# Kernel tuning notes

Measured on AMD Instinct MI355X. Metric: run time of the kernel, lower is better.

Reference implementation:

```python
import jax, jax.numpy as jnp
import numpy as np

# ---- structural constants (mirror e3nn SO3.tensor_productRs bookkeeping) ----
MUL = 2                      # multiplicity of every irrep in Rs_in / Rs_out
LS = [0, 1, 2]               # irrep orders present in Rs_in and Rs_out
L_MAX = 2                    # spherical-harmonics cutoff -> Y_dim = 9
N_BASIS, HIDDEN = 64, 64     # radial model sizes
R_MAX, GAMMA = 3.5, 4.0      # gaussian radial basis params


def _filter_paths():
    """One entry (l_filter) per (mul_out, mul_in, l_in, l_out, l_f) path."""
    paths = []
    for l_in in LS:
        for l_out in LS:
            for lf in range(abs(l_in - l_out), min(l_in + l_out, L_MAX) + 1):
                paths.extend([lf] * (MUL * MUL))  # mul_in * mul_out copies
    return paths  # len == n_path == 60


def _build_mix_matrices():
    """rf_mix[K, n_path]: broadcast each radial path weight over its 2l+1 components.
    ylm_mix[K, 9]: select Y_{l,m} for each filter component. Both 0/1, block sparse."""
    paths = _filter_paths()
    n_path = len(paths)
    K = sum(2 * l + 1 for l in paths)          # 204
    y_off = {0: 0, 1: 1, 2: 4}                 # offset of l-block inside Y (dim 9)
    rf = np.zeros((K, n_path), dtype=np.float32)
    ylm = np.zeros((K, 9), dtype=np.float32)
    k = 0
    for p, l in enumerate(paths):
        for m in range(2 * l + 1):
            rf[k, p] = 1.0
            ylm[k, y_off[l] + m] = 1.0
            k += 1
    return rf, ylm, n_path, K


def _sh_l012(n):
    """Real spherical harmonics l=0..2 on unit vectors n[Z,3] -> Y[9, Z]."""
    x, y, z = n[:, 0], n[:, 1], n[:, 2]
    c0 = 0.28209479177387814   # 1/(2 sqrt(pi))
    c1 = 0.4886025119029199    # sqrt(3/(4 pi))
    c2a = 1.0925484305920792   # sqrt(15/(4 pi))
    c2b = 0.31539156525252005  # sqrt(5/(16 pi))
    c2c = 0.5462742152960396   # sqrt(15/(16 pi))
    one = jnp.ones_like(x)
    return jnp.stack([
        c0 * one,
        c1 * y, c1 * z, c1 * x,
        c2a * x * y, c2a * y * z, c2b * (3.0 * z * z - 1.0), c2a * x * z,
        c2c * (x * x - y * y),
    ], axis=0)


def setup_inputs() -> dict:
    key = jax.random.key(0)
    k_r, k_cg, k_w1, k_w2 = jax.random.split(key, 4)
    Z = 65536
    D = MUL * sum(2 * l + 1 for l in LS)       # 18 (dim_in == dim_out)
    rf_np, ylm_np, n_path, K = _build_mix_matrices()
    r = 2.0 * jax.random.normal(k_r, (Z, 3), dtype=jnp.float32)
    cg = jax.random.normal(k_cg, (K, D, D), dtype=jnp.float32) / np.sqrt(K)
    W1 = jax.random.normal(k_w1, (N_BASIS, HIDDEN), dtype=jnp.float32) / np.sqrt(N_BASIS)
    b1 = jnp.zeros((HIDDEN,), dtype=jnp.float32)
    W2 = jax.random.normal(k_w2, (HIDDEN, n_path), dtype=jnp.float32) / np.sqrt(HIDDEN)
    b2 = jnp.zeros((n_path,), dtype=jnp.float32)
    return {"r": r, "W1": W1, "b1": b1, "W2": W2, "b2": b2,
            "cg": cg, "rf_mix": jnp.asarray(rf_np), "ylm_mix": jnp.asarray(ylm_np)}


def reference(r, W1, b1, W2, b2, cg, rf_mix, ylm_mix):
    radii = jnp.linalg.norm(r, axis=1)                    # [Z]
    n = r / (radii[:, None] + 1e-12)                      # unit directions
    Y = _sh_l012(n)                                       # [9, Z]  (sh returns [m, ...])
    centers = jnp.linspace(0.0, R_MAX, N_BASIS, dtype=jnp.float32)
    B = jnp.exp(-GAMMA * (radii[:, None] - centers) ** 2) # gaussian radial basis [Z, 64]
    R = jax.nn.relu(B @ W1 + b1) @ W2 + b2                # RadialModel -> [Z, n_path]
    Rm = jnp.einsum('kp,zp->zk', rf_mix, R)               # 'ij,zj->zi'
    Ym = jnp.einsum('ky,yz->zk', ylm_mix, Y)              # 'ij,jz->zi'
    # 'kij,zk,zk->zij' : fuse the two per-point vectors, then one GEMM over k
    kernel = jnp.einsum('kij,zk->zij', cg, Rm * Ym)       # [Z, 18, 18]
    return kernel
```

## Files before the change

kernel.cpp:

```cpp
#include <hip/hip_runtime.h>

#define NPATH 60
#define KDIM  204
#define KPAD  224
#define NIJ   324
#define NTIL  21
#define HID   64

typedef short bf16x8 __attribute__((ext_vector_type(8)));
typedef float f32x4  __attribute__((ext_vector_type(4)));

__device__ __align__(16) unsigned short g_w1s[4096];
__device__ __align__(16) unsigned short g_w2s[4096];
__device__ __align__(16) unsigned short g_cgs[75264];
__device__ unsigned char g_ptab[KDIM];
__device__ unsigned char g_ytab[KDIM];

__device__ inline unsigned short f2bf(float f) {
    unsigned int u = __builtin_bit_cast(unsigned int, f);
    u += 0x7fffu + ((u >> 16) & 1u);
    return (unsigned short)(u >> 16);
}
__device__ inline float bf2f(unsigned short h) {
    unsigned int u = ((unsigned int)h) << 16;
    return __builtin_bit_cast(float, u);
}

__global__ void prep_kernel(const float* __restrict__ W1, const float* __restrict__ W2,
                            const float* __restrict__ cg, const float* __restrict__ rf,
                            const float* __restrict__ ylm)
{
    int idx = blockIdx.x * 256 + threadIdx.x;
    if (idx < 4096) {
        int e = idx & 7, ln = (idx >> 3) & 63, nt = (idx >> 9) & 3, kc = idx >> 11;
        int k = kc * 32 + (ln >> 4) * 8 + e;
        int n = nt * 16 + (ln & 15);
        g_w1s[idx] = f2bf(W1[k * HID + n]);
    } else if (idx < 8192) {
        int j = idx - 4096;
        int e = j & 7, ln = (j >> 3) & 63, nt = (j >> 9) & 3, kc = j >> 11;
        int k = kc * 32 + (ln >> 4) * 8 + e;
        int n = nt * 16 + (ln & 15);
        g_w2s[j] = f2bf(n < NPATH ? W2[k * NPATH + n] : 0.0f);
    } else if (idx < 8192 + 75264) {
        int j = idx - 8192;
        int e = j & 7, ln = (j >> 3) & 63;
        int nt = (j >> 9) % NTIL;
        int kc = j / (512 * NTIL);
        int k = kc * 32 + (ln >> 4) * 8 + e;
        int n = nt * 16 + (ln & 15);
        g_cgs[j] = f2bf((k < KDIM && n < NIJ) ? cg[k * NIJ + n] : 0.0f);
    } else if (idx < 8192 + 75264 + KDIM) {
        int k = idx - (8192 + 75264);
        int p = 0, yy = 0;
        for (int q = 0; q < NPATH; q++) if (rf[k * NPATH + q] != 0.0f) p = q;
        for (int q = 0; q < 9; q++)     if (ylm[k * 9 + q]   != 0.0f) yy = q;
        g_ptab[k] = (unsigned char)p;
        g_ytab[k] = (unsigned char)yy;
    }
}

union SmemU {
    struct {
        unsigned short Blds[64][72];
        unsigned short Hlds[64][72];
    } p1;
    unsigned short Clds[64][228];
    float stage[16][340];
};

__global__ __launch_bounds__(256) void fused_kernel(
    const float* __restrict__ r, const float* __restrict__ b1,
    const float* __restrict__ b2, float* __restrict__ out)
{
    __shared__ SmemU sm;
    __shared__ unsigned short Rl[64][61];
    __shared__ float Yl[64][9];
    __shared__ float radl[64];
    __shared__ unsigned char ptabL[KDIM];
    __shared__ unsigned char ytabL[KDIM];

    const int tid  = threadIdx.x;
    const int wv   = tid >> 6;
    const int lane = tid & 63;
    const int quad = lane >> 4;
    const int l16  = lane & 15;
    const int z0   = blockIdx.x * 64;

    if (tid < 64) {
        int z = z0 + tid;
        float x = r[z * 3 + 0], y = r[z * 3 + 1], zc = r[z * 3 + 2];
        float rad = sqrtf(x * x + y * y + zc * zc);
        float inv = 1.0f / (rad + 1e-12f);
        float nx = x * inv, ny = y * inv, nz = zc * inv;
        radl[tid] = rad;
        const float c0 = 0.28209479177387814f, c1 = 0.4886025119029199f;
        const float c2a = 1.0925484305920792f, c2b = 0.31539156525252005f, c2c = 0.5462742152960396f;
        Yl[tid][0] = c0;
        Yl[tid][1] = c1 * ny;
        Yl[tid][2] = c1 * nz;
        Yl[tid][3] = c1 * nx;
        Yl[tid][4] = c2a * nx * ny;
        Yl[tid][5] = c2a * ny * nz;
        Yl[tid][6] = c2b * (3.0f * nz * nz - 1.0f);
        Yl[tid][7] = c2a * nx * nz;
        Yl[tid][8] = c2c * (nx * nx - ny * ny);
    }
    for (int k = tid; k < KDIM; k += 256) {
        ptabL[k] = g_ptab[k];
        ytabL[k] = g_ytab[k];
    }
    __syncthreads();

    {
        int zz = tid >> 2, grp = tid & 3;
        float rad = radl[zz];
        unsigned int* dst = (unsigned int*)&sm.p1.Blds[zz][grp * 16];
        const float step = 3.5f / 63.0f;
        #pragma unroll
        for (int ii = 0; ii < 8; ii++) {
            int i0 = grp * 16 + ii * 2;
            float d0 = rad - (float)i0 * step;
            float d1 = rad - (float)(i0 + 1) * step;
            unsigned int u0 = f2bf(expf(-4.0f * d0 * d0));
            unsigned int u1 = f2bf(expf(-4.0f * d1 * d1));
            dst[ii] = u0 | (u1 << 16);
        }
    }
    __syncthreads();

    {
        bf16x8 a0 = *(const bf16x8*)&sm.p1.Blds[wv * 16 + l16][0 + quad * 8];
        bf16x8 a1 = *(const bf16x8*)&sm.p1.Blds[wv * 16 + l16][32 + quad * 8];
        #pragma unroll
        for (int nt = 0; nt < 4; nt++) {
            bf16x8 bb0 = *(const bf16x8*)&g_w1s[((0 * 4 + nt) * 64 + lane) * 8];
            bf16x8 bb1 = *(const bf16x8*)&g_w1s[((1 * 4 + nt) * 64 + lane) * 8];
            f32x4 acc = {0.f, 0.f, 0.f, 0.f};
            acc = __builtin_amdgcn_mfma_f32_16x16x32_bf16(a0, bb0, acc, 0, 0, 0);
            acc = __builtin_amdgcn_mfma_f32_16x16x32_bf16(a1, bb1, acc, 0, 0, 0);
            int h = nt * 16 + l16;
            float bias = b1[h];
            #pragma unroll
            for (int rr = 0; rr < 4; rr++) {
                float v = acc[rr] + bias;
                v = v > 0.0f ? v : 0.0f;
                sm.p1.Hlds[wv * 16 + quad * 4 + rr][h] = f2bf(v);
            }
        }
    }
    __syncthreads();

    {
        bf16x8 a0 = *(const bf16x8*)&sm.p1.Hlds[wv * 16 + l16][0 + quad * 8];
        bf16x8 a1 = *(const bf16x8*)&sm.p1.Hlds[wv * 16 + l16][32 + quad * 8];
        #pragma unroll
        for (int nt = 0; nt < 4; nt++) {
            bf16x8 bb0 = *(const bf16x8*)&g_w2s[((0 * 4 + nt) * 64 + lane) * 8];
            bf16x8 bb1 = *(const bf16x8*)&g_w2s[((1 * 4 + nt) * 64 + lane) * 8];
            f32x4 acc = {0.f, 0.f, 0.f, 0.f};
            acc = __builtin_amdgcn_mfma_f32_16x16x32_bf16(a0, bb0, acc, 0, 0, 0);
            acc = __builtin_amdgcn_mfma_f32_16x16x32_bf16(a1, bb1, acc, 0, 0, 0);
            int p = nt * 16 + l16;
            if (p < NPATH) {
                float bias = b2[p];
                #pragma unroll
                for (int rr = 0; rr < 4; rr++)
                    Rl[wv * 16 + quad * 4 + rr][p] = f2bf(acc[rr] + bias);
            }
        }
    }
    __syncthreads();

    for (int idx = tid; idx < 64 * (KPAD / 2); idx += 256) {
        int z = idx / (KPAD / 2);
        int k = (idx % (KPAD / 2)) * 2;
        unsigned int u = 0;
        if (k < KDIM) {
            float cA = bf2f(Rl[z][ptabL[k]])     * Yl[z][ytabL[k]];
            float cB = bf2f(Rl[z][ptabL[k + 1]]) * Yl[z][ytabL[k + 1]];
            u = (unsigned int)f2bf(cA) | ((unsigned int)f2bf(cB) << 16);
        }
        *(unsigned int*)&sm.Clds[z][k] = u;
    }
    __syncthreads();

    const int ntb = wv * 5 + (wv > 0 ? 1 : 0);
    const int cnt = (wv == 0) ? 6 : 5;

    f32x4 acc[6][4];
    #pragma unroll
    for (int i = 0; i < 6; i++)
        #pragma unroll
        for (int zt = 0; zt < 4; zt++)
            acc[i][zt] = (f32x4){0.f, 0.f, 0.f, 0.f};

    #pragma unroll
    for (int kc = 0; kc < 7; kc++) {
        bf16x8 az[4];
        #pragma unroll
        for (int zt = 0; zt < 4; zt++)
            az[zt] = *(const bf16x8*)&sm.Clds[zt * 16 + l16][kc * 32 + quad * 8];

        bf16x8 bg[6];
        #pragma unroll
        for (int i = 0; i < 6; i++) {
            int nt = ntb + i; if (nt > NTIL - 1) nt = NTIL - 1;
            bg[i] = *(const bf16x8*)&g_cgs[((kc * NTIL + nt) * 64 + lane) * 8];
        }
        #pragma unroll
        for (int i = 0; i < 6; i++) {
            if (i < cnt) {
                #pragma unroll
                for (int zt = 0; zt < 4; zt++)
                    acc[i][zt] = __builtin_amdgcn_mfma_f32_16x16x32_bf16(az[zt], bg[i], acc[i][zt], 0, 0, 0);
            }
        }
    }

    for (int zt = 0; zt < 4; zt++) {
        __syncthreads();
        #pragma unroll
        for (int i = 0; i < 6; i++) {
            if (i < cnt) {
                int col = (ntb + i) * 16 + l16;
                #pragma unroll
                for (int rr = 0; rr < 4; rr++)
                    sm.stage[quad * 4 + rr][col] = acc[i][zt][rr];
            }
        }
        __syncthreads();
        for (int j = tid; j < 16 * (NIJ / 4); j += 256) {
            int row = j / (NIJ / 4);
            int c4  = j % (NIJ / 4);
            f32x4 v = *(const f32x4*)&sm.stage[row][c4 * 4];
            *(f32x4*)&out[(z0 + zt * 16 + row) * NIJ + c4 * 4] = v;
        }
    }
}

extern "C" void kernel_launch(void* const* d_in, const int* in_sizes, int n_in,
                              void* d_out, int out_size, void* d_ws, size_t ws_size,
                              hipStream_t stream) {
    const float* r   = (const float*)d_in[0];
    const float* W1  = (const float*)d_in[1];
    const float* b1  = (const float*)d_in[2];
    const float* W2  = (const float*)d_in[3];
    const float* b2  = (const float*)d_in[4];
    const float* cg  = (const float*)d_in[5];
    const float* rf  = (const float*)d_in[6];
    const float* ylm = (const float*)d_in[7];
    float* out = (float*)d_out;

    const int Z = in_sizes[0] / 3;

    prep_kernel<<<327, 256, 0, stream>>>(W1, W2, cg, rf, ylm);
    fused_kernel<<<Z / 64, 256, 0, stream>>>(r, b1, b2, out);
}
```

Measured before the change: 138.9 us.

## Store accumulators directly to global, pad LDS strides, use exp2 and fewer syncs

The output epilogue no longer stages each 16-row tile through a shared-memory buffer with two barriers per tile. Each lane now writes its MFMA accumulator values straight to global memory, which removes the staging buffer and its synchronisation but replaces 16-byte vector stores with scattered 4-byte stores. The B/H and C LDS row strides are padded to cut bank conflicts. The radius is recomputed per thread so the early barrier and the radl array go away, expf is replaced by the hardware exp2 with a prescaled constant, and launch bounds now request 4 blocks per CU.

```diff
diff --git a/kernel.cpp b/kernel.cpp
--- a/kernel.cpp
+++ b/kernel.cpp
@@ -6,6 +6,9 @@
 #define NIJ   324
 #define NTIL  21
 #define HID   64
+
+#define BHS   88
+#define CLS   232
 
 typedef short bf16x8 __attribute__((ext_vector_type(8)));
 typedef float f32x4  __attribute__((ext_vector_type(4)));
@@ -62,21 +65,19 @@
 
 union SmemU {
     struct {
-        unsigned short Blds[64][72];
-        unsigned short Hlds[64][72];
+        unsigned short Blds[64][BHS];
+        unsigned short Hlds[64][BHS];
     } p1;
-    unsigned short Clds[64][228];
-    float stage[16][340];
+    unsigned short Clds[64][CLS];
 };
 
-__global__ __launch_bounds__(256) void fused_kernel(
+__global__ __launch_bounds__(256, 4) void fused_kernel(
     const float* __restrict__ r, const float* __restrict__ b1,
     const float* __restrict__ b2, float* __restrict__ out)
 {
     __shared__ SmemU sm;
     __shared__ unsigned short Rl[64][61];
     __shared__ float Yl[64][9];
-    __shared__ float radl[64];
     __shared__ unsigned char ptabL[KDIM];
     __shared__ unsigned char ytabL[KDIM];
 
@@ -87,13 +88,16 @@
     const int l16  = lane & 15;
     const int z0   = blockIdx.x * 64;
 
+    for (int k = tid; k < KDIM; k += 256) {
+        ptabL[k] = g_ptab[k];
+        ytabL[k] = g_ytab[k];
+    }
     if (tid < 64) {
         int z = z0 + tid;
         float x = r[z * 3 + 0], y = r[z * 3 + 1], zc = r[z * 3 + 2];
         float rad = sqrtf(x * x + y * y + zc * zc);
         float inv = 1.0f / (rad + 1e-12f);
         float nx = x * inv, ny = y * inv, nz = zc * inv;
-        radl[tid] = rad;
         const float c0 = 0.28209479177387814f, c1 = 0.4886025119029199f;
         const float c2a = 1.0925484305920792f, c2b = 0.31539156525252005f, c2c = 0.5462742152960396f;
         Yl[tid][0] = c0;
@@ -106,24 +110,21 @@
         Yl[tid][7] = c2a * nx * nz;
         Yl[tid][8] = c2c * (nx * nx - ny * ny);
     }
-    for (int k = tid; k < KDIM; k += 256) {
-        ptabL[k] = g_ptab[k];
-        ytabL[k] = g_ytab[k];
-    }
-    __syncthreads();
-
     {
         int zz = tid >> 2, grp = tid & 3;
-        float rad = radl[zz];
+        int z = z0 + zz;
+        float x = r[z * 3 + 0], y = r[z * 3 + 1], zc = r[z * 3 + 2];
+        float rad = sqrtf(x * x + y * y + zc * zc);
+        const float step = 3.5f / 63.0f;
+        const float NL2E = -5.770780163555852f;
         unsigned int* dst = (unsigned int*)&sm.p1.Blds[zz][grp * 16];
-        const float step = 3.5f / 63.0f;
         #pragma unroll
         for (int ii = 0; ii < 8; ii++) {
             int i0 = grp * 16 + ii * 2;
             float d0 = rad - (float)i0 * step;
             float d1 = rad - (float)(i0 + 1) * step;
-            unsigned int u0 = f2bf(expf(-4.0f * d0 * d0));
-            unsigned int u1 = f2bf(expf(-4.0f * d1 * d1));
+            unsigned int u0 = f2bf(__builtin_amdgcn_exp2f(d0 * d0 * NL2E));
+            unsigned int u1 = f2bf(__builtin_amdgcn_exp2f(d1 * d1 * NL2E));
             dst[ii] = u0 | (u1 << 16);
         }
     }
@@ -218,23 +219,18 @@
         }
     }
 
-    for (int zt = 0; zt < 4; zt++) {
-        __syncthreads();
-        #pragma unroll
-        for (int i = 0; i < 6; i++) {
-            if (i < cnt) {
-                int col = (ntb + i) * 16 + l16;
+    #pragma unroll
+    for (int i = 0; i < 6; i++) {
+        if (i < cnt) {
+            int col = (ntb + i) * 16 + l16;
+            if (col < NIJ) {
                 #pragma unroll
-                for (int rr = 0; rr < 4; rr++)
-                    sm.stage[quad * 4 + rr][col] = acc[i][zt][rr];
-            }
-        }
-        __syncthreads();
-        for (int j = tid; j < 16 * (NIJ / 4); j += 256) {
-            int row = j / (NIJ / 4);
-            int c4  = j % (NIJ / 4);
-            f32x4 v = *(const f32x4*)&sm.stage[row][c4 * 4];
-            *(f32x4*)&out[(z0 + zt * 16 + row) * NIJ + c4 * 4] = v;
+                for (int zt = 0; zt < 4; zt++) {
+                    #pragma unroll
+                    for (int rr = 0; rr < 4; rr++)
+                        out[(z0 + zt * 16 + quad * 4 + rr) * NIJ + col] = acc[i][zt][rr];
+                }
+            }
         }
     }
 }
```

Result: slower. 162.7 us (+17.1%).
